# Kernel optimization log

Measured on AMD Instinct MI355X. Metric: run time of the kernel, lower is better.

Reference implementation:

```python
import jax, jax.numpy as jnp
import numpy as np

D_MODEL = 512
D_STATE = 16
D_CONV = 4
EXPAND = 2
HEADDIM = 64
D_INNER = EXPAND * D_MODEL            # 1024
NHEADS = D_INNER // HEADDIM           # 16
CONV_DIM = D_INNER + 2 * D_STATE      # 1056 (x, B, C channels)
D_IN_PROJ = 2 * D_INNER + 2 * D_STATE + NHEADS  # 2096
EPS = 1e-5
B_SZ, L_SEQ = 8, 4096


def _mamba_param_keys(prefix):
    return [prefix + n for n in
            ('in_proj', 'conv_w', 'conv_b', 'dt_bias', 'A_log', 'D', 'norm_w', 'out_proj')]


def _make_mamba_params(key, prefix):
    ks = jax.random.split(key, 4)
    s = 0.02
    return {
        prefix + 'in_proj': jax.random.normal(ks[0], (D_IN_PROJ, D_MODEL), jnp.float32) * s,
        prefix + 'conv_w': jax.random.normal(ks[1], (CONV_DIM, D_CONV), jnp.float32) * s,
        prefix + 'conv_b': jnp.zeros((CONV_DIM,), jnp.float32),
        prefix + 'dt_bias': jax.random.normal(ks[2], (NHEADS,), jnp.float32) * 0.1,
        prefix + 'A_log': jnp.log(jnp.arange(1, NHEADS + 1, dtype=jnp.float32)),
        prefix + 'D': jnp.ones((NHEADS,), jnp.float32),
        prefix + 'norm_w': jnp.ones((D_INNER,), jnp.float32),
        prefix + 'out_proj': jax.random.normal(ks[3], (D_MODEL, D_INNER), jnp.float32) * s,
    }


def setup_inputs() -> dict:
    key = jax.random.key(0)
    kx, kf, kb, kp = jax.random.split(key, 4)
    inp = {'x': jax.random.normal(kx, (B_SZ, L_SEQ, D_MODEL), jnp.float32)}
    inp.update(_make_mamba_params(kf, 'f_'))
    inp.update(_make_mamba_params(kb, 'b_'))
    kp1, kp2 = jax.random.split(kp)
    inp['proj_w'] = jax.random.normal(kp1, (D_MODEL, 2 * D_MODEL), jnp.float32) * 0.02
    inp['proj_b'] = jnp.zeros((D_MODEL,), jnp.float32)
    inp['ln_w'] = jnp.ones((D_MODEL,), jnp.float32)
    inp['ln_b'] = jnp.zeros((D_MODEL,), jnp.float32)
    return inp


def mamba2(x, in_proj, conv_w, conv_b, dt_bias, A_log, Dp, norm_w, out_proj):
    """Mamba2 block (ngroups=1): in_proj -> causal depthwise conv -> selective scan -> gated RMSNorm -> out_proj."""
    B, L, _ = x.shape
    zxbcdt = x @ in_proj.T                               # [B,L,2096]
    z = zxbcdt[..., :D_INNER]                            # gate
    xBC = zxbcdt[..., D_INNER:D_INNER + CONV_DIM]
    dt = jax.nn.softplus(zxbcdt[..., D_INNER + CONV_DIM:] + dt_bias)  # [B,L,H]
    # causal depthwise conv over (x, B, C) channels + SiLU
    xp = jnp.pad(xBC, ((0, 0), (D_CONV - 1, 0), (0, 0)))
    conv = conv_b + sum(xp[:, k:k + L, :] * conv_w[:, k] for k in range(D_CONV))
    xBC = jax.nn.silu(conv)
    xs = xBC[..., :D_INNER].reshape(B, L, NHEADS, HEADDIM)  # [B,L,H,P]
    Bm = xBC[..., D_INNER:D_INNER + D_STATE]                # [B,L,N]
    Cm = xBC[..., D_INNER + D_STATE:]                       # [B,L,N]
    A = -jnp.exp(A_log)                                     # [H]
    dA = jnp.exp(dt * A)                                    # [B,L,H]

    def step(h, inp):
        dA_t, dt_t, x_t, B_t, C_t = inp                     # [B,H],[B,H],[B,H,P],[B,N],[B,N]
        h = h * dA_t[..., None, None] + (dt_t[..., None] * x_t)[..., None] * B_t[:, None, None, :]
        y = jnp.einsum('bhpn,bn->bhp', h, C_t)
        return h, y

    h0 = jnp.zeros((B, NHEADS, HEADDIM, D_STATE), x.dtype)
    inps = (dA.transpose(1, 0, 2), dt.transpose(1, 0, 2), xs.transpose(1, 0, 2, 3),
            Bm.transpose(1, 0, 2), Cm.transpose(1, 0, 2))
    _, ys = jax.lax.scan(step, h0, inps)                    # ys: [L,B,H,P]
    y = ys.transpose(1, 0, 2, 3) + Dp[:, None] * xs         # skip connection
    y = y.reshape(B, L, D_INNER)
    # gated RMSNorm (norm_before_gate=False)
    y = y * jax.nn.silu(z)
    y = y * jax.lax.rsqrt(jnp.mean(y * y, axis=-1, keepdims=True) + EPS) * norm_w
    return y @ out_proj.T


def _layer_norm(x, w, b):
    mu = jnp.mean(x, axis=-1, keepdims=True)
    v = jnp.var(x, axis=-1, keepdims=True)
    return (x - mu) * jax.lax.rsqrt(v + EPS) * w + b


def reference(x,
              f_in_proj, f_conv_w, f_conv_b, f_dt_bias, f_A_log, f_D, f_norm_w, f_out_proj,
              b_in_proj, b_conv_w, b_conv_b, b_dt_bias, b_A_log, b_D, b_norm_w, b_out_proj,
              proj_w, proj_b, ln_w, ln_b):
    x_fwd = mamba2(x, f_in_proj, f_conv_w, f_conv_b, f_dt_bias, f_A_log, f_D, f_norm_w, f_out_proj)
    x_bwd = jnp.flip(
        mamba2(jnp.flip(x, axis=1), b_in_proj, b_conv_w, b_conv_b, b_dt_bias, b_A_log, b_D, b_norm_w, b_out_proj),
        axis=1)
    comb = jnp.concatenate([x_fwd, x_bwd], axis=-1)         # [B,L,2D]
    out = comb @ proj_w.T + proj_b                          # dropout is identity (eval / p=0)
    return _layer_norm(x + out, ln_w, ln_b)
```

## Files before the change

kernel.cpp:

```cpp
#include <hip/hip_runtime.h>
#include <hip/hip_bf16.h>
#include <math.h>

typedef __bf16 bf16x8_t __attribute__((ext_vector_type(8)));
typedef float f32x4_t __attribute__((ext_vector_type(4)));
typedef unsigned short u16x8_t __attribute__((ext_vector_type(8)));
typedef unsigned short u16x4_t __attribute__((ext_vector_type(4)));

#define DEV __device__ __forceinline__

DEV float bf2f(unsigned short u) {
    unsigned int v = ((unsigned int)u) << 16;
    return __builtin_bit_cast(float, v);
}
DEV unsigned short f2bf(float f) {
    unsigned int u = __builtin_bit_cast(unsigned int, f);
    u += 0x7fffu + ((u >> 16) & 1u);
    return (unsigned short)(u >> 16);
}

__global__ __launch_bounds__(256) void cvt_k(
    const float* __restrict__ in, unsigned short* __restrict__ out, int n8)
{
    int t = blockIdx.x * 256 + threadIdx.x;
    if (t >= n8) return;
    f32x4_t a = ((const f32x4_t*)in)[t * 2];
    f32x4_t b = ((const f32x4_t*)in)[t * 2 + 1];
    u16x8_t o;
#pragma unroll
    for (int j = 0; j < 4; j++) { o[j] = f2bf(a[j]); o[4 + j] = f2bf(b[j]); }
    ((u16x8_t*)out)[t] = o;
}

template <int NT, bool FLIP_A, bool FLIP_C, bool OUT_F32, bool ADD_BIAS, bool ACCUM>
__global__ __launch_bounds__(256, 2) void gemm_bt(
    const unsigned short* __restrict__ A,
    const unsigned short* __restrict__ W,
    void* __restrict__ Cout,
    const float* __restrict__ bias,
    int N, int K, int ldc, int col_ofs)
{
    __shared__ __attribute__((aligned(16))) unsigned char smem[16384];
    const int tid  = threadIdx.x;
    const int wave = tid >> 6;
    const int lane = tid & 63;

    int mtile_i, ntile_i;
    if (NT == 0) {
        mtile_i = blockIdx.y;
        ntile_i = blockIdx.x;
    } else {
        const int L = blockIdx.x;
        const int MTl = (int)gridDim.x / NT;
        const int ppx = MTl >> 3;
        const int xcd = L & 7, q = L >> 3;
        mtile_i = xcd * ppx + q / NT;
        ntile_i = q % NT;
    }
    const int mtile = mtile_i << 7;
    const int ntile = ntile_i << 7;

    const int c0 = tid, c1 = 256 + tid;
    const int r0 = c0 >> 2, p0 = c0 & 3, g0 = p0 ^ ((r0 >> 1) & 3);
    const int r1 = c1 >> 2, p1 = c1 & 3, g1 = p1 ^ ((r1 >> 1) & 3);

    int am0 = mtile + r0; if (FLIP_A) am0 ^= 4095;
    int am1 = mtile + r1; if (FLIP_A) am1 ^= 4095;
    const unsigned short* aP0 = A + (size_t)am0 * K + g0 * 8;
    const unsigned short* aP1 = A + (size_t)am1 * K + g1 * 8;

    int wr0 = ntile + r0; if (wr0 > N - 1) wr0 = N - 1;
    int wr1 = ntile + r1; if (wr1 > N - 1) wr1 = N - 1;
    const unsigned short* wP0 = W + (size_t)wr0 * K + g0 * 8;
    const unsigned short* wP1 = W + (size_t)wr1 * K + g1 * 8;

    unsigned char* ldsA = smem;
    unsigned char* ldsW = smem + 8192;
    unsigned char* ldsA0 = ldsA + wave * 1024;
    unsigned char* ldsA1 = ldsA + 4096 + wave * 1024;
    unsigned char* ldsW0 = ldsW + wave * 1024;
    unsigned char* ldsW1 = ldsW + 4096 + wave * 1024;

    f32x4_t acc[4][4] = {};

    const int wm = (wave & 1) << 6;
    const int wn = (wave >> 1) << 6;
    const int r    = lane & 15;
    const int quad = lane >> 4;
    const int sw   = (r >> 1) & 3;

    int aoff[4], woff[4];
#pragma unroll
    for (int i = 0; i < 4; i++) {
        int m = wm + i * 16 + r;
        aoff[i] = (m * 4 + (quad ^ sw)) * 16;
        int n = wn + i * 16 + r;
        woff[i] = (n * 4 + (quad ^ sw)) * 16;
    }

    for (int k0 = 0; k0 < K; k0 += 32) {
        __builtin_amdgcn_global_load_lds(
            (const __attribute__((address_space(1))) void*)(aP0 + k0),
            (__attribute__((address_space(3))) void*)ldsA0, 16, 0, 0);
        __builtin_amdgcn_global_load_lds(
            (const __attribute__((address_space(1))) void*)(aP1 + k0),
            (__attribute__((address_space(3))) void*)ldsA1, 16, 0, 0);
        __builtin_amdgcn_global_load_lds(
            (const __attribute__((address_space(1))) void*)(wP0 + k0),
            (__attribute__((address_space(3))) void*)ldsW0, 16, 0, 0);
        __builtin_amdgcn_global_load_lds(
            (const __attribute__((address_space(1))) void*)(wP1 + k0),
            (__attribute__((address_space(3))) void*)ldsW1, 16, 0, 0);
        __syncthreads();

        bf16x8_t af[4], wf[4];
#pragma unroll
        for (int i = 0; i < 4; i++)
            af[i] = __builtin_bit_cast(bf16x8_t, *(const u16x8_t*)(ldsA + aoff[i]));
#pragma unroll
        for (int j = 0; j < 4; j++)
            wf[j] = __builtin_bit_cast(bf16x8_t, *(const u16x8_t*)(ldsW + woff[j]));
#pragma unroll
        for (int i = 0; i < 4; i++)
#pragma unroll
            for (int j = 0; j < 4; j++)
                acc[i][j] = __builtin_amdgcn_mfma_f32_16x16x32_bf16(af[i], wf[j], acc[i][j], 0, 0, 0);
        __syncthreads();
    }

#pragma unroll
    for (int i = 0; i < 4; i++) {
#pragma unroll
        for (int j = 0; j < 4; j++) {
            int cc = ntile + wn + j * 16 + r;
            if (cc >= N) continue;
#pragma unroll
            for (int reg = 0; reg < 4; reg++) {
                int rr = mtile + wm + i * 16 + quad * 4 + reg;
                int orow = FLIP_C ? (rr ^ 4095) : rr;
                float v = acc[i][j][reg];
                if (ADD_BIAS) v += bias[cc];
                if (OUT_F32) {
                    float* p = (float*)Cout + (size_t)orow * ldc + col_ofs + cc;
                    if (ACCUM) v += *p;
                    *p = v;
                } else {
                    ((unsigned short*)Cout)[(size_t)orow * ldc + col_ofs + cc] = f2bf(v);
                }
            }
        }
    }
}

__global__ __launch_bounds__(256) void pack_pw_k(
    const float* __restrict__ pw, unsigned short* __restrict__ pwb)
{
    int t = blockIdx.x * 256 + threadIdx.x;
    int j8 = t & 63;
    int n  = (t >> 6) & 511;
    int dir = t >> 15;
    const float* src = pw + (size_t)n * 1024 + dir * 512 + j8 * 8;
    f32x4_t a = *(const f32x4_t*)src;
    f32x4_t b = *(const f32x4_t*)(src + 4);
    u16x8_t o;
#pragma unroll
    for (int j = 0; j < 4; j++) { o[j] = f2bf(a[j]); o[4 + j] = f2bf(b[j]); }
    *(u16x8_t*)(pwb + (size_t)dir * 512 * 512 + (size_t)n * 512 + j8 * 8) = o;
}

__global__ __launch_bounds__(256) void tr_op_k(
    const float* __restrict__ op0, const float* __restrict__ op1,
    unsigned short* __restrict__ opT)
{
    __shared__ float tile[32][33];
    const int dir = blockIdx.z;
    const float* op = dir ? op1 : op0;
    const int k0 = blockIdx.x * 32;
    const int j0 = blockIdx.y * 32;
    const int tx = threadIdx.x & 31, ty = threadIdx.x >> 5;
#pragma unroll
    for (int i = 0; i < 4; i++) {
        int j = j0 + ty + i * 8;
        tile[ty + i * 8][tx] = op[(size_t)j * 1024 + k0 + tx];
    }
    __syncthreads();
    unsigned short* dst = opT + (size_t)dir * 1024 * 512;
#pragma unroll
    for (int i = 0; i < 4; i++) {
        int k = k0 + ty + i * 8;
        dst[(size_t)k * 512 + j0 + tx] = f2bf(tile[tx][ty + i * 8]);
    }
}

__global__ __launch_bounds__(256) void conv_silu_k(
    const unsigned short* __restrict__ xin,
    const float* __restrict__ cw,
    const float* __restrict__ cb,
    unsigned short* __restrict__ outp)
{
    int t = blockIdx.x * 256 + threadIdx.x;
    int c8 = t % 132;
    int rb = t / 132;
    int c = c8 * 8;
    int row0 = rb * 8;
    int l0 = row0 & 4095;

    float w[8][4];
#pragma unroll
    for (int j = 0; j < 8; j++) {
        f32x4_t wv = *(const f32x4_t*)(cw + (c + j) * 4);
        w[j][0] = wv[0]; w[j][1] = wv[1]; w[j][2] = wv[2]; w[j][3] = wv[3];
    }
    float bia[8];
    {
        f32x4_t b0 = *(const f32x4_t*)(cb + c);
        f32x4_t b1 = *(const f32x4_t*)(cb + c + 4);
#pragma unroll
        for (int j = 0; j < 4; j++) { bia[j] = b0[j]; bia[4 + j] = b1[j]; }
    }

    u16x8_t zero;
#pragma unroll
    for (int j = 0; j < 8; j++) zero[j] = 0;

    u16x8_t win[11];
#pragma unroll
    for (int u = 0; u < 11; u++) {
        int lu = l0 - 3 + u;
        win[u] = (lu >= 0)
            ? *(const u16x8_t*)(xin + (size_t)(row0 - 3 + u) * 1072 + c)
            : zero;
    }

#pragma unroll
    for (int s = 0; s < 8; s++) {
        float acc[8];
#pragma unroll
        for (int j = 0; j < 8; j++) acc[j] = bia[j];
#pragma unroll
        for (int k = 0; k < 4; k++) {
            u16x8_t xv = win[s + k];
#pragma unroll
            for (int j = 0; j < 8; j++)
                acc[j] = fmaf(bf2f(xv[j]), w[j][k], acc[j]);
        }
        u16x8_t o;
#pragma unroll
        for (int j = 0; j < 8; j++) {
            float xx = acc[j];
            o[j] = f2bf(xx * __builtin_amdgcn_rcpf(1.f + __expf(-xx)));
        }
        *(u16x8_t*)(outp + (size_t)(row0 + s) * 1056 + c) = o;
    }
}

__global__ __launch_bounds__(256) void dt_pre_k(
    const unsigned short* __restrict__ xin,
    const float* __restrict__ dt_bias,
    const float* __restrict__ A_log,
    float* __restrict__ dtb, float* __restrict__ ldab)
{
    int t = blockIdx.x * 256 + threadIdx.x;
    int h = t & 15;
    int row = t >> 4;
    float x = bf2f(xin[(size_t)row * 1072 + 1056 + h]) + dt_bias[h];
    float dt = (x > 20.f) ? x : log1pf(__expf(x));
    float A = -__expf(A_log[h]);
    dtb[t] = dt;
    ldab[t] = dt * A;
}

DEV void stage_xt(const unsigned short* __restrict__ xrow, unsigned short* XtW, int l)
{
    u16x8_t xv[8];
#pragma unroll
    for (int m = 0; m < 8; m++) xv[m] = *(const u16x8_t*)(xrow + m * 8);
#pragma unroll
    for (int p = 0; p < 64; p++) {
        int blkc = (l >> 3) ^ (p & 7);
        XtW[p * 64 + blkc * 8 + (l & 7)] = xv[p >> 3][p & 7];
    }
}

DEV bf16x8_t xt_frag(const unsigned short* XtW, int r, int quad, int jj, int kk)
{
    int p = jj * 16 + r;
    int blkc = (kk * 4 + quad) ^ (p & 7);
    return __builtin_bit_cast(bf16x8_t, *(const u16x8_t*)(XtW + p * 64 + blkc * 8));
}

__global__ __launch_bounds__(256) void scan_chstate_k(
    const unsigned short* __restrict__ xc,
    const float* __restrict__ dtb,
    float* __restrict__ lcs,
    float* __restrict__ Hend, float* __restrict__ dec)
{
    __shared__ __attribute__((aligned(16))) unsigned char sm[37120];
    unsigned short* Btr = (unsigned short*)sm;
    float* csW = (float*)(sm + 2304);
    float* dtW = (float*)(sm + 3328);
    unsigned short* Xt0 = (unsigned short*)(sm + 4352);

    const int tid = threadIdx.x;
    const int w = tid >> 6, l = tid & 63;
    const int r = l & 15, quad = l >> 4;
    const int row0 = blockIdx.x * 64;
    const int b = blockIdx.x >> 6, chunk = blockIdx.x & 63;
    const int h = blockIdx.y * 4 + w;
    const int blk = ((b * 16 + h) << 6) | chunk;

    {
        int n = tid & 15, s0 = (tid >> 4) * 4;
#pragma unroll
        for (int js = 0; js < 4; js++) {
            int s = s0 + js;
            Btr[n * 72 + s] = xc[(size_t)(row0 + s) * 1056 + 1024 + n];
        }
    }

    float v   = lcs[(size_t)(row0 + l) * 16 + h];
    float dtv = dtb[(size_t)(row0 + l) * 16 + h];
#pragma unroll
    for (int d = 1; d < 64; d <<= 1) {
        float o = __shfl_up(v, d, 64);
        if (l >= d) v += o;
    }
    lcs[(size_t)(row0 + l) * 16 + h] = v;
    csW[w * 64 + l] = v;
    dtW[w * 64 + l] = dtv;
    if (l == 63) dec[blk] = __expf(v);
    __syncthreads();

    unsigned short* XtW = Xt0 + w * 4096;
    stage_xt(xc + (size_t)(row0 + l) * 1056 + h * 64, XtW, l);

    const float* csr = csW + w * 64;
    const float* dtr = dtW + w * 64;
    float cs63 = csr[63];

    f32x4_t z = {0.f, 0.f, 0.f, 0.f};
    f32x4_t hacc[4] = {z, z, z, z};
#pragma unroll
    for (int kk = 0; kk < 2; kk++) {
        int sb = kk * 32 + quad * 8;
        u16x8_t bv = *(const u16x8_t*)(Btr + r * 72 + sb);
        f32x4_t c0 = *(const f32x4_t*)(csr + sb);
        f32x4_t c1 = *(const f32x4_t*)(csr + sb + 4);
        f32x4_t d0 = *(const f32x4_t*)(dtr + sb);
        f32x4_t d1 = *(const f32x4_t*)(dtr + sb + 4);
        u16x8_t wv;
#pragma unroll
        for (int j = 0; j < 4; j++) {
            wv[j]     = f2bf(bf2f(bv[j])     * d0[j] * __expf(cs63 - c0[j]));
            wv[4 + j] = f2bf(bf2f(bv[4 + j]) * d1[j] * __expf(cs63 - c1[j]));
        }
        bf16x8_t wf = __builtin_bit_cast(bf16x8_t, wv);
#pragma unroll
        for (int jj = 0; jj < 4; jj++)
            hacc[jj] = __builtin_amdgcn_mfma_f32_16x16x32_bf16(wf, xt_frag(XtW, r, quad, jj, kk), hacc[jj], 0, 0, 0);
    }
    float* o = Hend + (size_t)blk * 1024;
#pragma unroll
    for (int jj = 0; jj < 4; jj++)
#pragma unroll
        for (int reg = 0; reg < 4; reg++)
            o[(jj * 16 + r) * 16 + quad * 4 + reg] = hacc[jj][reg];
}

__global__ __launch_bounds__(64) void scan_comb_k(float* __restrict__ H, const float* __restrict__ dec)
{
    int bh = blockIdx.x >> 2;
    int q  = blockIdx.x & 3;
    int t  = threadIdx.x;
    float* base = H + (size_t)bh * 64 * 1024 + q * 256 + t * 4;
    const float* dp = dec + bh * 64;
    f32x4_t hs = {0.f, 0.f, 0.f, 0.f};
    f32x4_t cur = *(const f32x4_t*)base;
    for (int c = 0; c < 64; c++) {
        int cn = (c < 63) ? c + 1 : 63;
        f32x4_t nxt = *(const f32x4_t*)(base + (size_t)cn * 1024);
        float d = dp[c];
        *(f32x4_t*)(base + (size_t)c * 1024) = hs;
#pragma unroll
        for (int j = 0; j < 4; j++) hs[j] = fmaf(hs[j], d, cur[j]);
        cur = nxt;
    }
}

__global__ __launch_bounds__(256) void scan_chout_k(
    const unsigned short* __restrict__ xc,
    const float* __restrict__ dtb, const float* __restrict__ csb,
    const float* __restrict__ Hst, const float* __restrict__ Dp,
    unsigned short* __restrict__ ybuf)
{
    __shared__ __attribute__((aligned(16))) unsigned char sm[60416];
    unsigned short* Ct = (unsigned short*)sm;
    unsigned short* Bt = (unsigned short*)(sm + 4096);
    float* S   = (float*)(sm + 8192);
    float* csL = (float*)(sm + 25600);
    float* dtL = (float*)(sm + 26624);
    unsigned short* Xt0 = (unsigned short*)(sm + 27648);

    const int tid = threadIdx.x;
    const int w = tid >> 6, l = tid & 63;
    const int r = l & 15, quad = l >> 4;
    const int row0 = blockIdx.x * 64;
    const int b = blockIdx.x >> 6, chunk = blockIdx.x & 63;
    const int h = blockIdx.y * 4 + w;
    const int blk = ((b * 16 + h) << 6) | chunk;

    {
        int rowi = tid >> 2, seg = tid & 3;
        u16x8_t vb, vc;
        if (seg < 2) {
            const unsigned short* src = xc + (size_t)(row0 + rowi) * 1056 + 1024 + seg * 8;
            vb = *(const u16x8_t*)src;
            vc = *(const u16x8_t*)(src + 16);
        } else {
#pragma unroll
            for (int j = 0; j < 8; j++) { vb[j] = 0; vc[j] = 0; }
        }
        *(u16x8_t*)(Bt + rowi * 32 + seg * 8) = vb;
        *(u16x8_t*)(Ct + rowi * 32 + seg * 8) = vc;
    }
    csL[w * 64 + l] = csb[(size_t)(row0 + l) * 16 + h];
    dtL[w * 64 + l] = dtb[(size_t)(row0 + l) * 16 + h];
    __syncthreads();

    {
        bf16x8_t cf = __builtin_bit_cast(bf16x8_t, *(const u16x8_t*)(Ct + (w * 16 + r) * 32 + quad * 8));
        f32x4_t z = {0.f, 0.f, 0.f, 0.f};
#pragma unroll
        for (int j = 0; j < 4; j++) {
            bf16x8_t bfv = __builtin_bit_cast(bf16x8_t, *(const u16x8_t*)(Bt + (j * 16 + r) * 32 + quad * 8));
            f32x4_t d = __builtin_amdgcn_mfma_f32_16x16x32_bf16(cf, bfv, z, 0, 0, 0);
#pragma unroll
            for (int reg = 0; reg < 4; reg++)
                S[(w * 16 + quad * 4 + reg) * 68 + j * 16 + r] = d[reg];
        }
    }
    __syncthreads();

    unsigned short* XtW = Xt0 + w * 4096;
    stage_xt(xc + (size_t)(row0 + l) * 1056 + h * 64, XtW, l);

    const float* csr = csL + w * 64;
    const float* dtr = dtL + w * 64;

    f32x4_t acc[4][4];
    {
        bf16x8_t hf[4];
#pragma unroll
        for (int jj = 0; jj < 4; jj++) {
            int p = jj * 16 + r;
            u16x8_t hv;
            if (quad < 2) {
                const float* hp = Hst + (size_t)blk * 1024 + p * 16 + quad * 8;
                f32x4_t h0 = *(const f32x4_t*)hp;
                f32x4_t h1 = *(const f32x4_t*)(hp + 4);
#pragma unroll
                for (int j = 0; j < 4; j++) { hv[j] = f2bf(h0[j]); hv[4 + j] = f2bf(h1[j]); }
            } else {
#pragma unroll
                for (int j = 0; j < 8; j++) hv[j] = 0;
            }
            hf[jj] = __builtin_bit_cast(bf16x8_t, hv);
        }
        f32x4_t z = {0.f, 0.f, 0.f, 0.f};
#pragma unroll
        for (int i = 0; i < 4; i++) {
            bf16x8_t cf = __builtin_bit_cast(bf16x8_t, *(const u16x8_t*)(Ct + (i * 16 + r) * 32 + quad * 8));
#pragma unroll
            for (int jj = 0; jj < 4; jj++)
                acc[i][jj] = __builtin_amdgcn_mfma_f32_16x16x32_bf16(cf, hf[jj], z, 0, 0, 0);
        }
#pragma unroll
        for (int i = 0; i < 4; i++) {
            f32x4_t es;
#pragma unroll
            for (int reg = 0; reg < 4; reg++) es[reg] = __expf(csr[i * 16 + quad * 4 + reg]);
#pragma unroll
            for (int jj = 0; jj < 4; jj++)
#pragma unroll
                for (int reg = 0; reg < 4; reg++) acc[i][jj][reg] *= es[reg];
        }
    }

#pragma unroll
    for (int kk = 0; kk < 2; kk++) {
        int sb = kk * 32 + quad * 8;
        bf16x8_t xf[4];
#pragma unroll
        for (int jj = 0; jj < 4; jj++) xf[jj] = xt_frag(XtW, r, quad, jj, kk);
        f32x4_t c0 = *(const f32x4_t*)(csr + sb);
        f32x4_t c1 = *(const f32x4_t*)(csr + sb + 4);
        f32x4_t d0 = *(const f32x4_t*)(dtr + sb);
        f32x4_t d1 = *(const f32x4_t*)(dtr + sb + 4);
#pragma unroll
        for (int i = 0; i < 4; i++) {
            int t = i * 16 + r;
            float cst = csr[t];
            const float* Srow = S + t * 68;
            f32x4_t s0 = *(const f32x4_t*)(Srow + sb);
            f32x4_t s1 = *(const f32x4_t*)(Srow + sb + 4);
            u16x8_t wv;
#pragma unroll
            for (int j = 0; j < 4; j++) {
                int s = sb + j;
                float v0 = (s <= t) ? __expf(cst - c0[j]) * d0[j] * s0[j] : 0.f;
                wv[j] = f2bf(v0);
                int s2 = sb + 4 + j;
                float v1 = (s2 <= t) ? __expf(cst - c1[j]) * d1[j] * s1[j] : 0.f;
                wv[4 + j] = f2bf(v1);
            }
            bf16x8_t wf = __builtin_bit_cast(bf16x8_t, wv);
#pragma unroll
            for (int jj = 0; jj < 4; jj++)
                acc[i][jj] = __builtin_amdgcn_mfma_f32_16x16x32_bf16(wf, xf[jj], acc[i][jj], 0, 0, 0);
        }
    }

    float Dh = Dp[h];
#pragma unroll
    for (int i = 0; i < 4; i++) {
#pragma unroll
        for (int jj = 0; jj < 4; jj++) {
            int p = jj * 16 + r;
            int t0 = i * 16 + quad * 4;
            int blk2 = (t0 >> 3) ^ (p & 7);
            u16x4_t x4 = *(const u16x4_t*)(XtW + p * 64 + blk2 * 8 + (t0 & 7));
#pragma unroll
            for (int reg = 0; reg < 4; reg++) {
                float yv = fmaf(Dh, bf2f(x4[reg]), acc[i][jj][reg]);
                ybuf[(size_t)(row0 + t0 + reg) * 1024 + h * 64 + p] = f2bf(yv);
            }
        }
    }
}

__global__ __launch_bounds__(256) void rmsgate_k(
    unsigned short* __restrict__ y,
    const unsigned short* __restrict__ z,
    const float* __restrict__ nw)
{
    const int wave = threadIdx.x >> 6, lane = threadIdx.x & 63;
    const size_t row = (size_t)blockIdx.x * 4 + wave;
    const int c = lane * 16;
    unsigned short* yp = y + row * 1024 + c;
    const unsigned short* zp = z + row * 1024 + c;
    u16x8_t yv0 = *(const u16x8_t*)yp;
    u16x8_t yv1 = *(const u16x8_t*)(yp + 8);
    u16x8_t zv0 = *(const u16x8_t*)zp;
    u16x8_t zv1 = *(const u16x8_t*)(zp + 8);
    float g[16];
    float ss = 0.f;
#pragma unroll
    for (int j = 0; j < 8; j++) {
        float zf = bf2f(zv0[j]);
        float sil = zf * __builtin_amdgcn_rcpf(1.f + __expf(-zf));
        g[j] = bf2f(yv0[j]) * sil;
        ss += g[j] * g[j];
    }
#pragma unroll
    for (int j = 0; j < 8; j++) {
        float zf = bf2f(zv1[j]);
        float sil = zf * __builtin_amdgcn_rcpf(1.f + __expf(-zf));
        g[8 + j] = bf2f(yv1[j]) * sil;
        ss += g[8 + j] * g[8 + j];
    }
#pragma unroll
    for (int m = 32; m > 0; m >>= 1) ss += __shfl_xor(ss, m, 64);
    float scale = rsqrtf(ss * (1.f / 1024.f) + 1e-5f);
    f32x4_t w0 = *(const f32x4_t*)(nw + c);
    f32x4_t w1 = *(const f32x4_t*)(nw + c + 4);
    f32x4_t w2 = *(const f32x4_t*)(nw + c + 8);
    f32x4_t w3 = *(const f32x4_t*)(nw + c + 12);
    u16x8_t o0, o1;
#pragma unroll
    for (int j = 0; j < 4; j++) {
        o0[j]     = f2bf(g[j]      * scale * w0[j]);
        o0[4 + j] = f2bf(g[4 + j]  * scale * w1[j]);
        o1[j]     = f2bf(g[8 + j]  * scale * w2[j]);
        o1[4 + j] = f2bf(g[12 + j] * scale * w3[j]);
    }
    *(u16x8_t*)yp = o0;
    *(u16x8_t*)(yp + 8) = o1;
}

__global__ __launch_bounds__(256) void ln_k(
    const float* __restrict__ x,
    const float* __restrict__ f,
    const float* __restrict__ lw,
    const float* __restrict__ lb,
    float* __restrict__ outp)
{
    const int wave = threadIdx.x >> 6, lane = threadIdx.x & 63;
    const size_t row = (size_t)blockIdx.x * 4 + wave;
    const int c = lane * 8;
    f32x4_t xv0 = *(const f32x4_t*)(x + row * 512 + c);
    f32x4_t xv1 = *(const f32x4_t*)(x + row * 512 + c + 4);
    f32x4_t fv0 = *(const f32x4_t*)(f + row * 512 + c);
    f32x4_t fv1 = *(const f32x4_t*)(f + row * 512 + c + 4);
    float s[8];
    float sum = 0.f, sq = 0.f;
#pragma unroll
    for (int j = 0; j < 4; j++) {
        s[j] = xv0[j] + fv0[j];
        s[4 + j] = xv1[j] + fv1[j];
    }
#pragma unroll
    for (int j = 0; j < 8; j++) { sum += s[j]; sq += s[j] * s[j]; }
#pragma unroll
    for (int m = 32; m > 0; m >>= 1) {
        sum += __shfl_xor(sum, m, 64);
        sq  += __shfl_xor(sq, m, 64);
    }
    float mu = sum * (1.f / 512.f);
    float var = sq * (1.f / 512.f) - mu * mu;
    if (var < 0.f) var = 0.f;
    float inv = rsqrtf(var + 1e-5f);
    f32x4_t w0 = *(const f32x4_t*)(lw + c);
    f32x4_t w1 = *(const f32x4_t*)(lw + c + 4);
    f32x4_t b0 = *(const f32x4_t*)(lb + c);
    f32x4_t b1 = *(const f32x4_t*)(lb + c + 4);
    f32x4_t o0, o1;
#pragma unroll
    for (int j = 0; j < 4; j++) {
        o0[j] = (s[j] - mu) * inv * w0[j] + b0[j];
        o1[j] = (s[4 + j] - mu) * inv * w1[j] + b1[j];
    }
    *(f32x4_t*)(outp + row * 512 + c) = o0;
    *(f32x4_t*)(outp + row * 512 + c + 4) = o1;
}

extern "C" void kernel_launch(void* const* d_in, const int* in_sizes, int n_in,
                              void* d_out, int out_size, void* d_ws, size_t ws_size,
                              hipStream_t stream)
{
    (void)in_sizes; (void)n_in; (void)out_size;

    const float* x           = (const float*)d_in[0];
    const float* in_proj[2]  = {(const float*)d_in[1],  (const float*)d_in[9]};
    const float* conv_w[2]   = {(const float*)d_in[2],  (const float*)d_in[10]};
    const float* conv_b[2]   = {(const float*)d_in[3],  (const float*)d_in[11]};
    const float* dt_bias[2]  = {(const float*)d_in[4],  (const float*)d_in[12]};
    const float* A_log[2]    = {(const float*)d_in[5],  (const float*)d_in[13]};
    const float* Dp[2]       = {(const float*)d_in[6],  (const float*)d_in[14]};
    const float* norm_w[2]   = {(const float*)d_in[7],  (const float*)d_in[15]};
    const float* out_proj[2] = {(const float*)d_in[8],  (const float*)d_in[16]};
    const float* proj_w      = (const float*)d_in[17];
    const float* proj_b      = (const float*)d_in[18];
    const float* ln_w        = (const float*)d_in[19];
    const float* ln_b        = (const float*)d_in[20];
    float* outp = (float*)d_out;

    const size_t IP_ELEMS = (size_t)2096 * 512;
    const size_t X_ELEMS  = (size_t)32768 * 512;

    const size_t constBytes = X_ELEMS * 2 + 2 * IP_ELEMS * 2 + 2 * 512 * 1024 * 2
                            + 2 * 512 * 512 * 2 + 2 * 1024 * 512 * 2 + 8192;
    int g = 1;
    {
        const int cands[3] = {8, 4, 2};
        for (int ci = 0; ci < 3; ci++) {
            size_t R = (size_t)cands[ci] * 4096;
            size_t need = constBytes + R * (2144 + 2112 + 2048 + 64 + 64 + 1024)
                        + (size_t)cands[ci] * 1024 * 4 + 16 * 256;
            if (need <= ws_size) { g = cands[ci]; break; }
        }
    }
    const size_t R = (size_t)g * 4096;
    const int nGroups = 8 / g;
    const int MT = (int)(R >> 7);

    char* ws = (char*)d_ws;
    size_t off = 0;
    auto alloc = [&](size_t bytes) -> char* {
        char* p = ws + off;
        off += (bytes + 255) & ~(size_t)255;
        return p;
    };
    unsigned short* xb16  = (unsigned short*)alloc(X_ELEMS * 2);
    unsigned short* ipb16[2];
    ipb16[0] = (unsigned short*)alloc(IP_ELEMS * 2);
    ipb16[1] = (unsigned short*)alloc(IP_ELEMS * 2);
    unsigned short* Ebuf  = (unsigned short*)alloc(2 * 512 * 1024 * 2);
    unsigned short* Ef    = Ebuf;
    unsigned short* Eb    = Ebuf + 512 * 1024;
    unsigned short* pwb   = (unsigned short*)alloc(2 * 512 * 512 * 2);
    unsigned short* opT   = (unsigned short*)alloc(2 * 1024 * 512 * 2);
    unsigned short* xbcdt = (unsigned short*)alloc(R * 1072 * 2);
    unsigned short* ybuf  = xbcdt;
    unsigned short* xconv = (unsigned short*)alloc(R * 1056 * 2);
    unsigned short* zbuf  = xconv;
    float* fbuf = (float*)alloc(R * 512 * 4);
    float* dtb  = (float*)alloc(R * 16 * 4);
    float* dab  = (float*)alloc(R * 16 * 4);
    float* Hbuf = (float*)alloc(R * 1024);
    float* dec  = (float*)alloc((size_t)g * 1024 * 4);

    dim3 blk(256);

    cvt_k<<<(unsigned)((X_ELEMS / 8 + 255) / 256), blk, 0, stream>>>(x, xb16, (int)(X_ELEMS / 8));
    cvt_k<<<(unsigned)((IP_ELEMS / 8 + 255) / 256), blk, 0, stream>>>(in_proj[0], ipb16[0], (int)(IP_ELEMS / 8));
    cvt_k<<<(unsigned)((IP_ELEMS / 8 + 255) / 256), blk, 0, stream>>>(in_proj[1], ipb16[1], (int)(IP_ELEMS / 8));
    pack_pw_k<<<256, blk, 0, stream>>>(proj_w, pwb);
    tr_op_k<<<dim3(32, 16, 2), blk, 0, stream>>>(out_proj[0], out_proj[1], opT);
    gemm_bt<0, false, false, false, false, false><<<dim3(8, 4), blk, 0, stream>>>(
        pwb, opT, Ef, nullptr, 1024, 512, 1024, 0);
    gemm_bt<0, false, false, false, false, false><<<dim3(8, 4), blk, 0, stream>>>(
        pwb + 512 * 512, opT + 1024 * 512, Eb, nullptr, 1024, 512, 1024, 0);

    for (int grp = 0; grp < nGroups; grp++) {
        const unsigned short* xg = xb16 + (size_t)grp * R * 512;
        const float* xgf = x + (size_t)grp * R * 512;
        float* og = outp + (size_t)grp * R * 512;

        for (int dir = 0; dir < 2; dir++) {
            if (dir == 0)
                gemm_bt<9, false, false, false, false, false><<<(unsigned)(9 * MT), blk, 0, stream>>>(
                    xg, ipb16[0] + (size_t)1024 * 512, xbcdt, nullptr, 1072, 512, 1072, 0);
            else
                gemm_bt<9, true, false, false, false, false><<<(unsigned)(9 * MT), blk, 0, stream>>>(
                    xg, ipb16[1] + (size_t)1024 * 512, xbcdt, nullptr, 1072, 512, 1072, 0);

            conv_silu_k<<<(unsigned)(R * 132 / 2048), blk, 0, stream>>>(xbcdt, conv_w[dir], conv_b[dir], xconv);
            dt_pre_k<<<(unsigned)(R * 16 / 256), blk, 0, stream>>>(xbcdt, dt_bias[dir], A_log[dir], dtb, dab);

            scan_chstate_k<<<dim3((unsigned)(R / 64), 4), blk, 0, stream>>>(xconv, dtb, dab, Hbuf, dec);
            scan_comb_k<<<(unsigned)(g * 64), dim3(64), 0, stream>>>(Hbuf, dec);
            scan_chout_k<<<dim3((unsigned)(R / 64), 4), blk, 0, stream>>>(xconv, dtb, dab, Hbuf, Dp[dir], ybuf);

            if (dir == 0)
                gemm_bt<8, false, false, false, false, false><<<(unsigned)(8 * MT), blk, 0, stream>>>(
                    xg, ipb16[0], zbuf, nullptr, 1024, 512, 1024, 0);
            else
                gemm_bt<8, true, false, false, false, false><<<(unsigned)(8 * MT), blk, 0, stream>>>(
                    xg, ipb16[1], zbuf, nullptr, 1024, 512, 1024, 0);

            rmsgate_k<<<(unsigned)(R / 4), blk, 0, stream>>>(ybuf, zbuf, norm_w[dir]);

            if (dir == 0)
                gemm_bt<4, false, false, true, true, false><<<(unsigned)(4 * MT), blk, 0, stream>>>(
                    ybuf, Ef, fbuf, proj_b, 512, 1024, 512, 0);
            else
                gemm_bt<4, false, true, true, false, true><<<(unsigned)(4 * MT), blk, 0, stream>>>(
                    ybuf, Eb, fbuf, nullptr, 512, 1024, 512, 0);
        }
        ln_k<<<(unsigned)(R / 4), blk, 0, stream>>>(xgf, fbuf, ln_w, ln_b, og);
    }
}
```

Baseline: 911.6 us.

## Double-buffer LDS tiles in bf16 GEMM to overlap global loads with MFMA

The GEMM kernel now uses two LDS stages instead of one. Each iteration issues the global_load_lds prefetch of the next K-slice into the alternate buffer before running the MFMAs on the current one. The aim is to hide global-memory latency behind compute instead of loading and computing in strict alternation. It doubles the LDS footprint per block to 32KB and relies on the barrier's implicit wait on outstanding loads, which may reduce occupancy or serialize anyway.

```diff
diff --git a/kernel.cpp b/kernel.cpp
--- a/kernel.cpp
+++ b/kernel.cpp
@@ -40,7 +40,7 @@
     const float* __restrict__ bias,
     int N, int K, int ldc, int col_ofs)
 {
-    __shared__ __attribute__((aligned(16))) unsigned char smem[16384];
+    __shared__ __attribute__((aligned(16))) unsigned char smem[32768];
     const int tid  = threadIdx.x;
     const int wave = tid >> 6;
     const int lane = tid & 63;
@@ -74,12 +74,7 @@
     const unsigned short* wP0 = W + (size_t)wr0 * K + g0 * 8;
     const unsigned short* wP1 = W + (size_t)wr1 * K + g1 * 8;
 
-    unsigned char* ldsA = smem;
-    unsigned char* ldsW = smem + 8192;
-    unsigned char* ldsA0 = ldsA + wave * 1024;
-    unsigned char* ldsA1 = ldsA + 4096 + wave * 1024;
-    unsigned char* ldsW0 = ldsW + wave * 1024;
-    unsigned char* ldsW1 = ldsW + 4096 + wave * 1024;
+    const int stago = wave * 1024;
 
     f32x4_t acc[4][4] = {};
 
@@ -95,31 +90,42 @@
         int m = wm + i * 16 + r;
         aoff[i] = (m * 4 + (quad ^ sw)) * 16;
         int n = wn + i * 16 + r;
-        woff[i] = (n * 4 + (quad ^ sw)) * 16;
-    }
-
-    for (int k0 = 0; k0 < K; k0 += 32) {
+        woff[i] = (n * 4 + (quad ^ sw)) * 16 + 8192;
+    }
+
+    auto STAGE = [&](int kt, int bufsel) {
+        const int k0 = kt << 5;
+        unsigned char* base = smem + bufsel * 16384;
         __builtin_amdgcn_global_load_lds(
             (const __attribute__((address_space(1))) void*)(aP0 + k0),
-            (__attribute__((address_space(3))) void*)ldsA0, 16, 0, 0);
+            (__attribute__((address_space(3))) void*)(base + stago), 16, 0, 0);
         __builtin_amdgcn_global_load_lds(
             (const __attribute__((address_space(1))) void*)(aP1 + k0),
-            (__attribute__((address_space(3))) void*)ldsA1, 16, 0, 0);
+            (__attribute__((address_space(3))) void*)(base + 4096 + stago), 16, 0, 0);
         __builtin_amdgcn_global_load_lds(
             (const __attribute__((address_space(1))) void*)(wP0 + k0),
-            (__attribute__((address_space(3))) void*)ldsW0, 16, 0, 0);
+            (__attribute__((address_space(3))) void*)(base + 8192 + stago), 16, 0, 0);
         __builtin_amdgcn_global_load_lds(
             (const __attribute__((address_space(1))) void*)(wP1 + k0),
-            (__attribute__((address_space(3))) void*)ldsW1, 16, 0, 0);
-        __syncthreads();
-
+            (__attribute__((address_space(3))) void*)(base + 12288 + stago), 16, 0, 0);
+    };
+
+    const int nt = K >> 5;
+    STAGE(0, 0);
+    __syncthreads();
+
+    for (int kt = 0; kt < nt; kt++) {
+        const int cur = kt & 1;
+        if (kt + 1 < nt) STAGE(kt + 1, cur ^ 1);
+
+        const unsigned char* bufc = smem + cur * 16384;
         bf16x8_t af[4], wf[4];
 #pragma unroll
         for (int i = 0; i < 4; i++)
-            af[i] = __builtin_bit_cast(bf16x8_t, *(const u16x8_t*)(ldsA + aoff[i]));
+            af[i] = __builtin_bit_cast(bf16x8_t, *(const u16x8_t*)(bufc + aoff[i]));
 #pragma unroll
         for (int j = 0; j < 4; j++)
-            wf[j] = __builtin_bit_cast(bf16x8_t, *(const u16x8_t*)(ldsW + woff[j]));
+            wf[j] = __builtin_bit_cast(bf16x8_t, *(const u16x8_t*)(bufc + woff[j]));
 #pragma unroll
         for (int i = 0; i < 4; i++)
 #pragma unroll
```

Measured after the change: 876.9 us. -3.8%, faster.
